# Performance work log

Hardware: AMD Instinct MI355X
Metric: run time of the kernel (lower is better)

## Reference

```python
import jax, jax.numpy as jnp
import numpy as np

D = 1024  # d_model

# default_syb decomposed statically (forward called with syb=None, pre_train=False):
# rows 0-4:   single nets: net'0' on idx [0,1,2]; net'1' on idx 6; net'2' on idx 6
# rows 5-18:  double net '0' on index pairs below
# rows 19-21: single net '3' on idx [0,1,2]
SINGLE_GROUPS = [(0, [0, 1, 2]), (1, [6]), (2, [6])]  # nets for rows 0-4
DOUBLE_PAIRS = np.array([[0,3],[0,4],[0,5],[0,6],[1,3],[1,4],[1,5],[1,6],
                         [2,3],[2,4],[2,5],[2,6],[4,5],[4,6]])  # rows 5-18
TAIL_SINGLE = (3, [0, 1, 2])  # rows 19-21


def setup_inputs() -> dict:
    key = jax.random.key(0)
    ks = jax.random.split(key, 16)
    bs = 4096
    s = 1.0 / np.sqrt(D)
    feat = jax.random.normal(ks[0], (bs, 7, D), dtype=jnp.float32)
    # 4 single-expert 2-layer MLPs: Linear(D,D) -> ReLU -> Linear(D,2)
    sw1 = jax.random.normal(ks[1], (4, D, D), dtype=jnp.float32) * s
    sb1 = jax.random.normal(ks[2], (4, D), dtype=jnp.float32) * 0.01
    sw2 = jax.random.normal(ks[3], (4, D, 2), dtype=jnp.float32) * s
    sb2 = jax.random.normal(ks[4], (4, 2), dtype=jnp.float32) * 0.01
    # 1 double-expert MLP: Linear(2D,D) -> ReLU -> Linear(D,2)
    dw1 = jax.random.normal(ks[5], (2 * D, D), dtype=jnp.float32) * s
    db1 = jax.random.normal(ks[6], (D,), dtype=jnp.float32) * 0.01
    dw2 = jax.random.normal(ks[7], (D, 2), dtype=jnp.float32) * s
    db2 = jax.random.normal(ks[8], (2,), dtype=jnp.float32) * 0.01
    return {"feat": feat, "sw1": sw1, "sb1": sb1, "sw2": sw2, "sb2": sb2,
            "dw1": dw1, "db1": db1, "dw2": dw2, "db2": db2}


def _mlp(x, w1, b1, w2, b2):
    return jax.nn.relu(x @ w1 + b1) @ w2 + b2


def reference(feat, sw1, sb1, sw2, sb2, dw1, db1, dw2, db2):
    # feat: [B, 7, D] -> out [B, 22, 2], rows ordered as default_syb
    parts = []
    for net, idxs in SINGLE_GROUPS:  # rows 0-4
        g = feat[:, jnp.array(idxs)]                     # [B, n, D]
        parts.append(_mlp(g, sw1[net], sb1[net], sw2[net], sb2[net]))
    i1 = jnp.asarray(DOUBLE_PAIRS[:, 0]); i2 = jnp.asarray(DOUBLE_PAIRS[:, 1])
    pair = jnp.concatenate([feat[:, i1], feat[:, i2]], axis=-1)  # [B, 14, 2D]
    parts.append(_mlp(pair, dw1, db1, dw2, db2))         # rows 5-18
    net, idxs = TAIL_SINGLE                               # rows 19-21
    g = feat[:, jnp.array(idxs)]
    parts.append(_mlp(g, sw1[net], sb1[net], sw2[net], sb2[net]))
    return jnp.concatenate(parts, axis=1)                 # [B, 22, 2]
```

## Files before the change

### kernel.cpp

```cpp
#include <hip/hip_runtime.h>
#include <hip/hip_bf16.h>
#include <stdint.h>


typedef __attribute__((ext_vector_type(4))) float f32x4;
typedef __attribute__((ext_vector_type(8))) short short8;
typedef __attribute__((ext_vector_type(8))) __bf16 bf16x8;

__device__ inline unsigned short f2bf(float f) {
  union { float f; uint32_t u; } x; x.f = f;
  uint32_t u = x.u;
  return (unsigned short)((u + 0x7fffu + ((u >> 16) & 1u)) >> 16);
}

__global__ void init_out(float* __restrict__ out,
                         const float* __restrict__ sb2,
                         const float* __restrict__ db2) {
  int i = blockIdx.x * 256 + threadIdx.x;
  if (i >= 180224) return;
  int c = i & 1;
  int p = (i >> 1) % 22;
  float v;
  if (p < 3)       v = sb2[0 + c];
  else if (p == 3) v = sb2[2 + c];
  else if (p == 4) v = sb2[4 + c];
  else if (p < 19) v = db2[c];
  else             v = sb2[6 + c];
  out[i] = v;
}

__global__ void prep_weights(const float* __restrict__ sw1,
                             const float* __restrict__ dw1,
                             unsigned short* __restrict__ wp) {
  int c = blockIdx.x * 256 + threadIdx.x;
  const float* W;
  size_t ob;
  int local;
  if (c < 524288) {
    int net = c >> 17;
    local = c & 131071;
    W = sw1 + (size_t)net * 1048576;
    ob = (size_t)net * 1048576;
  } else {
    local = c - 524288;
    W = dw1;
    ob = 4194304;
  }
  int c2 = local & 2047;
  int tile = local >> 11;
  int ct = tile & 3;
  int kstep = tile >> 2;
  int kk = c2 >> 10, nblk = (c2 >> 6) & 15, kgrp = (c2 >> 4) & 3, j15 = c2 & 15;
  int kb = kstep * 64 + kk * 32 + kgrp * 8;
  int j = ct * 256 + nblk * 16 + j15;
  short8 v;
#pragma unroll
  for (int e = 0; e < 8; e++) v[e] = (short)f2bf(W[(size_t)(kb + e) * 1024 + j]);
  *(short8*)(wp + ob + (size_t)local * 8) = v;
}

__global__ void prep_feat(const float* __restrict__ feat,
                          unsigned short* __restrict__ fb) {
  int i = blockIdx.x * 256 + threadIdx.x;
  const float* s = feat + (size_t)i * 8;
  f32x4 a = *(const f32x4*)s;
  f32x4 b = *(const f32x4*)(s + 4);
  short8 v;
  v[0] = (short)f2bf(a[0]); v[1] = (short)f2bf(a[1]);
  v[2] = (short)f2bf(a[2]); v[3] = (short)f2bf(a[3]);
  v[4] = (short)f2bf(b[0]); v[5] = (short)f2bf(b[1]);
  v[6] = (short)f2bf(b[2]); v[7] = (short)f2bf(b[3]);
  *(short8*)(fb + (size_t)i * 8) = v;
}

__global__ __launch_bounds__(256) void fused_main(
    const float* __restrict__ sb1, const float* __restrict__ sw2,
    const float* __restrict__ db1, const float* __restrict__ dw2,
    const unsigned short* __restrict__ wp,
    const unsigned short* __restrict__ fb, float* __restrict__ out) {
  __shared__ short8 Abuf[512];
  __shared__ short8 Bbuf[2048];

  const int tid = threadIdx.x;
  const int lane = tid & 63;
  const int wid = tid >> 6;
  const int r15 = lane & 15;

  const int bid = blockIdx.x;
  const int swz = (bid & 7) * 704 + (bid >> 3);
  const int ct = swz & 3;
  const int rt = swz >> 2;

  int task, nsteps, rbase;
  const unsigned short* wpt;
  const float* b1;
  const float* w2;
  if (rt < 192)       { task = 0; rbase = rt * 64;          wpt = wp;           b1 = sb1;        w2 = sw2;        nsteps = 16; }
  else if (rt < 256)  { task = 1; rbase = (rt - 192) * 64;  wpt = wp + 1048576; b1 = sb1 + 1024; w2 = sw2 + 2048; nsteps = 16; }
  else if (rt < 320)  { task = 2; rbase = (rt - 256) * 64;  wpt = wp + 2097152; b1 = sb1 + 2048; w2 = sw2 + 4096; nsteps = 16; }
  else if (rt < 1216) { task = 3; rbase = (rt - 320) * 64;  wpt = wp + 4194304; b1 = db1;        w2 = dw2;        nsteps = 32; }
  else                { task = 4; rbase = (rt - 1216) * 64; wpt = wp + 3145728; b1 = sb1 + 3072; w2 = sw2 + 6144; nsteps = 16; }

  const unsigned short *p0, *p1;
  {
    int arow = rbase + wid * 16 + r15;
    int ab, as1, as2;
    if (task == 0 || task == 4) {
      ab = arow / 3; int s = arow - ab * 3; as1 = s; as2 = s;
    } else if (task == 3) {
      ab = arow / 14; int pp = arow - ab * 14;
      if (pp < 12) { as1 = pp >> 2; as2 = 3 + (pp & 3); }
      else         { as1 = 4;       as2 = (pp == 12) ? 5 : 6; }
    } else {
      ab = arow; as1 = 6; as2 = 6;
    }
    int kl = (lane >> 4) * 8;
    p0 = fb + ((size_t)ab * 7 + as1) * 1024 + kl;
    p1 = fb + ((size_t)ab * 7 + as2) * 1024 + kl;
  }

  f32x4 acc[4][4] = {};

  for (int ks = 0; ks < nsteps; ks++) {
    const int ko = (ks & 15) * 64;
    const unsigned short* a = (ks < 16) ? p0 : p1;
    __builtin_amdgcn_global_load_lds(
        (const __attribute__((address_space(1))) void*)(a + ko),
        (__attribute__((address_space(3))) void*)((char*)Abuf + wid * 1024),
        16, 0, 0);
    __builtin_amdgcn_global_load_lds(
        (const __attribute__((address_space(1))) void*)(a + ko + 32),
        (__attribute__((address_space(3))) void*)((char*)Abuf + 4096 + wid * 1024),
        16, 0, 0);
    const unsigned short* wsrc = wpt + (size_t)(ks * 4 + ct) * 16384;
#pragma unroll
    for (int i = 0; i < 8; i++) {
      __builtin_amdgcn_global_load_lds(
          (const __attribute__((address_space(1))) void*)(wsrc + i * 2048 + tid * 8),
          (__attribute__((address_space(3))) void*)((char*)Bbuf + i * 4096 + wid * 1024),
          16, 0, 0);
    }
    __syncthreads();
#pragma unroll
    for (int kk = 0; kk < 2; kk++) {
      short8 afr[4], bfr[4];
#pragma unroll
      for (int m = 0; m < 4; m++)
        afr[m] = Abuf[kk * 256 + m * 64 + (lane >> 4) * 16 + r15];
#pragma unroll
      for (int n = 0; n < 4; n++)
        bfr[n] = Bbuf[kk * 1024 + (wid * 4 + n) * 64 + (lane >> 4) * 16 + r15];
#pragma unroll
      for (int m = 0; m < 4; m++)
#pragma unroll
        for (int n = 0; n < 4; n++)
          acc[m][n] = __builtin_amdgcn_mfma_f32_16x16x32_bf16(
              __builtin_bit_cast(bf16x8, afr[m]),
              __builtin_bit_cast(bf16x8, bfr[n]), acc[m][n], 0, 0, 0);
    }
    __syncthreads();
  }

  float b1v[4], w20v[4], w21v[4];
#pragma unroll
  for (int n = 0; n < 4; n++) {
    int j = ct * 256 + wid * 64 + n * 16 + r15;
    b1v[n] = b1[j];
    w20v[n] = w2[2 * j];
    w21v[n] = w2[2 * j + 1];
  }
#pragma unroll
  for (int m = 0; m < 4; m++) {
#pragma unroll
    for (int r = 0; r < 4; r++) {
      float s0 = 0.f, s1 = 0.f;
#pragma unroll
      for (int n = 0; n < 4; n++) {
        float h = acc[m][n][r] + b1v[n];
        h = fmaxf(h, 0.f);
        s0 = fmaf(h, w20v[n], s0);
        s1 = fmaf(h, w21v[n], s1);
      }
#pragma unroll
      for (int off = 1; off < 16; off <<= 1) {
        s0 += __shfl_xor(s0, off, 64);
        s1 += __shfl_xor(s1, off, 64);
      }
      if (r15 == 0) {
        int rg = rbase + m * 16 + (lane >> 4) * 4 + r;
        int b, p;
        if (task == 0)      { b = rg / 3;  p = rg - b * 3; }
        else if (task == 1) { b = rg;      p = 3; }
        else if (task == 2) { b = rg;      p = 4; }
        else if (task == 3) { b = rg / 14; p = 5 + (rg - b * 14); }
        else                { b = rg / 3;  p = 19 + (rg - b * 3); }
        atomicAdd(out + ((size_t)b * 44 + p * 2), s0);
        atomicAdd(out + ((size_t)b * 44 + p * 2 + 1), s1);
      }
    }
  }
}

extern "C" void kernel_launch(void* const* d_in, const int* in_sizes, int n_in,
                              void* d_out, int out_size, void* d_ws, size_t ws_size,
                              hipStream_t stream) {
  const float* feat = (const float*)d_in[0];
  const float* sw1  = (const float*)d_in[1];
  const float* sb1  = (const float*)d_in[2];
  const float* sw2  = (const float*)d_in[3];
  const float* sb2  = (const float*)d_in[4];
  const float* dw1  = (const float*)d_in[5];
  const float* db1  = (const float*)d_in[6];
  const float* dw2  = (const float*)d_in[7];
  const float* db2  = (const float*)d_in[8];
  float* out = (float*)d_out;
  unsigned short* wp = (unsigned short*)d_ws;
  unsigned short* fb = wp + 6291456;

  init_out<<<704, 256, 0, stream>>>(out, sb2, db2);
  prep_weights<<<3072, 256, 0, stream>>>(sw1, dw1, wp);
  prep_feat<<<14336, 256, 0, stream>>>(feat, fb);
  fused_main<<<5632, 256, 0, stream>>>(sb1, sw2, db1, dw2, wp, fb, out);
}
```

Measured before the change: 490.8 us.

## Double-buffer LDS tiles and remap block-to-task swizzle across XCDs

```diff
diff --git a/kernel.cpp b/kernel.cpp
--- a/kernel.cpp
+++ b/kernel.cpp
@@ -78,28 +78,32 @@
     const float* __restrict__ db1, const float* __restrict__ dw2,
     const unsigned short* __restrict__ wp,
     const unsigned short* __restrict__ fb, float* __restrict__ out) {
-  __shared__ short8 Abuf[512];
-  __shared__ short8 Bbuf[2048];
+  __shared__ short8 Abuf0[512];
+  __shared__ short8 Abuf1[512];
+  __shared__ short8 Bbuf0[2048];
+  __shared__ short8 Bbuf1[2048];
 
   const int tid = threadIdx.x;
   const int lane = tid & 63;
   const int wid = tid >> 6;
   const int r15 = lane & 15;
+  const int fr = (lane >> 4) * 16 + r15;
 
   const int bid = blockIdx.x;
-  const int swz = (bid & 7) * 704 + (bid >> 3);
-  const int ct = swz & 3;
-  const int rt = swz >> 2;
-
-  int task, nsteps, rbase;
+  const int x = bid & 7;
+  const int j = bid >> 3;
+
+  int task, nsteps, v;
   const unsigned short* wpt;
   const float* b1;
   const float* w2;
-  if (rt < 192)       { task = 0; rbase = rt * 64;          wpt = wp;           b1 = sb1;        w2 = sw2;        nsteps = 16; }
-  else if (rt < 256)  { task = 1; rbase = (rt - 192) * 64;  wpt = wp + 1048576; b1 = sb1 + 1024; w2 = sw2 + 2048; nsteps = 16; }
-  else if (rt < 320)  { task = 2; rbase = (rt - 256) * 64;  wpt = wp + 2097152; b1 = sb1 + 2048; w2 = sw2 + 4096; nsteps = 16; }
-  else if (rt < 1216) { task = 3; rbase = (rt - 320) * 64;  wpt = wp + 4194304; b1 = db1;        w2 = dw2;        nsteps = 32; }
-  else                { task = 4; rbase = (rt - 1216) * 64; wpt = wp + 3145728; b1 = sb1 + 3072; w2 = sw2 + 6144; nsteps = 16; }
+  if (j < 96)       { task = 0; v = x * 96 + j;         wpt = wp;           b1 = sb1;        w2 = sw2;        nsteps = 16; }
+  else if (j < 128) { task = 1; v = x * 32 + (j - 96);  wpt = wp + 1048576; b1 = sb1 + 1024; w2 = sw2 + 2048; nsteps = 16; }
+  else if (j < 160) { task = 2; v = x * 32 + (j - 128); wpt = wp + 2097152; b1 = sb1 + 2048; w2 = sw2 + 4096; nsteps = 16; }
+  else if (j < 608) { task = 3; v = x * 448 + (j - 160); wpt = wp + 4194304; b1 = db1;       w2 = dw2;        nsteps = 32; }
+  else              { task = 4; v = x * 96 + (j - 608); wpt = wp + 3145728; b1 = sb1 + 3072; w2 = sw2 + 6144; nsteps = 16; }
+  const int ct = v & 3;
+  const int rbase = (v >> 2) * 64;
 
   const unsigned short *p0, *p1;
   {
@@ -121,53 +125,70 @@
 
   f32x4 acc[4][4] = {};
 
-  for (int ks = 0; ks < nsteps; ks++) {
-    const int ko = (ks & 15) * 64;
-    const unsigned short* a = (ks < 16) ? p0 : p1;
-    __builtin_amdgcn_global_load_lds(
-        (const __attribute__((address_space(1))) void*)(a + ko),
-        (__attribute__((address_space(3))) void*)((char*)Abuf + wid * 1024),
-        16, 0, 0);
-    __builtin_amdgcn_global_load_lds(
-        (const __attribute__((address_space(1))) void*)(a + ko + 32),
-        (__attribute__((address_space(3))) void*)((char*)Abuf + 4096 + wid * 1024),
-        16, 0, 0);
-    const unsigned short* wsrc = wpt + (size_t)(ks * 4 + ct) * 16384;
-#pragma unroll
-    for (int i = 0; i < 8; i++) {
-      __builtin_amdgcn_global_load_lds(
-          (const __attribute__((address_space(1))) void*)(wsrc + i * 2048 + tid * 8),
-          (__attribute__((address_space(3))) void*)((char*)Bbuf + i * 4096 + wid * 1024),
-          16, 0, 0);
-    }
+#define STAGE(KS, AB, BB)                                                     \
+  do {                                                                        \
+    const int ko_ = ((KS) & 15) * 64;                                         \
+    const unsigned short* a_ = ((KS) < 16) ? p0 : p1;                         \
+    __builtin_amdgcn_global_load_lds(                                         \
+        (const __attribute__((address_space(1))) void*)(a_ + ko_),            \
+        (__attribute__((address_space(3))) void*)((char*)(AB) + wid * 1024),  \
+        16, 0, 0);                                                            \
+    __builtin_amdgcn_global_load_lds(                                         \
+        (const __attribute__((address_space(1))) void*)(a_ + ko_ + 32),       \
+        (__attribute__((address_space(3))) void*)((char*)(AB) + 4096 + wid * 1024), \
+        16, 0, 0);                                                            \
+    const unsigned short* ws_ = wpt + (size_t)((KS) * 4 + ct) * 16384;        \
+    _Pragma("unroll")                                                         \
+    for (int i_ = 0; i_ < 8; i_++) {                                          \
+      __builtin_amdgcn_global_load_lds(                                       \
+          (const __attribute__((address_space(1))) void*)(ws_ + i_ * 2048 + tid * 8), \
+          (__attribute__((address_space(3))) void*)((char*)(BB) + i_ * 4096 + wid * 1024), \
+          16, 0, 0);                                                          \
+    }                                                                         \
+  } while (0)
+
+#define COMPUTE(AB, BB)                                                       \
+  do {                                                                        \
+    _Pragma("unroll")                                                         \
+    for (int kk_ = 0; kk_ < 2; kk_++) {                                       \
+      short8 afr[4], bfr[4];                                                  \
+      _Pragma("unroll")                                                       \
+      for (int m_ = 0; m_ < 4; m_++)                                          \
+        afr[m_] = (AB)[kk_ * 256 + m_ * 64 + fr];                             \
+      _Pragma("unroll")                                                       \
+      for (int n_ = 0; n_ < 4; n_++)                                          \
+        bfr[n_] = (BB)[kk_ * 1024 + (wid * 4 + n_) * 64 + fr];                \
+      _Pragma("unroll")                                                       \
+      for (int m_ = 0; m_ < 4; m_++)                                          \
+        _Pragma("unroll")                                                     \
+        for (int n_ = 0; n_ < 4; n_++)                                        \
+          acc[m_][n_] = __builtin_amdgcn_mfma_f32_16x16x32_bf16(              \
+              __builtin_bit_cast(bf16x8, afr[m_]),                            \
+              __builtin_bit_cast(bf16x8, bfr[n_]), acc[m_][n_], 0, 0, 0);     \
+    }                                                                         \
+  } while (0)
+
+  STAGE(0, Abuf0, Bbuf0);
+  __syncthreads();
+
+  for (int ks = 0; ks < nsteps; ks += 2) {
+    STAGE(ks + 1, Abuf1, Bbuf1);
+    COMPUTE(Abuf0, Bbuf0);
     __syncthreads();
-#pragma unroll
-    for (int kk = 0; kk < 2; kk++) {
-      short8 afr[4], bfr[4];
-#pragma unroll
-      for (int m = 0; m < 4; m++)
-        afr[m] = Abuf[kk * 256 + m * 64 + (lane >> 4) * 16 + r15];
-#pragma unroll
-      for (int n = 0; n < 4; n++)
-        bfr[n] = Bbuf[kk * 1024 + (wid * 4 + n) * 64 + (lane >> 4) * 16 + r15];
-#pragma unroll
-      for (int m = 0; m < 4; m++)
-#pragma unroll
-        for (int n = 0; n < 4; n++)
-          acc[m][n] = __builtin_amdgcn_mfma_f32_16x16x32_bf16(
-              __builtin_bit_cast(bf16x8, afr[m]),
-              __builtin_bit_cast(bf16x8, bfr[n]), acc[m][n], 0, 0, 0);
-    }
+    if (ks + 2 < nsteps) STAGE(ks + 2, Abuf0, Bbuf0);
+    COMPUTE(Abuf1, Bbuf1);
     __syncthreads();
   }
+#undef STAGE
+#undef COMPUTE
 
   float b1v[4], w20v[4], w21v[4];
 #pragma unroll
   for (int n = 0; n < 4; n++) {
-    int j = ct * 256 + wid * 64 + n * 16 + r15;
-    b1v[n] = b1[j];
-    w20v[n] = w2[2 * j];
-    w21v[n] = w2[2 * j + 1];
+    int jj = ct * 256 + wid * 64 + n * 16 + r15;
+    b1v[n] = b1[jj];
+    w20v[n] = w2[2 * jj];
+    w21v[n] = w2[2 * jj + 1];
   }
 #pragma unroll
   for (int m = 0; m < 4; m++) {
```

Result: slower. 547.8 us (+11.6%).
